# Optimization experiments

Hardware: AMD Instinct MI355X
Metric: run time of the kernel (lower is better)

The kernel has to match this reference:

```python
import jax, jax.numpy as jnp
import numpy as np

D = 64      # size_in
RANK = 4    # rank
N = 262144  # batch of samples


def setup_inputs() -> dict:
    key = jax.random.key(0)
    k1, k2, k3, k4, k5 = jax.random.split(key, 5)
    s1 = 1.0 / np.sqrt(D)        # torch Linear init bound for linear1 (in=D)
    s2 = 1.0 / np.sqrt(2 * D)    # bound for linear2 (in=2D)
    return {
        "t": jnp.zeros((1,), dtype=jnp.float32),
        "input_": jax.random.normal(k1, (N, 2 * D), dtype=jnp.float32),
        "W1": jax.random.uniform(k2, (2 * D, D), jnp.float32, -s1, s1),
        "b1": jax.random.uniform(k3, (2 * D,), jnp.float32, -s1, s1),
        "W2": jax.random.uniform(k4, (RANK * D, 2 * D), jnp.float32, -s2, s2),
        "b2": jax.random.uniform(k5, (RANK * D,), jnp.float32, -s2, s2),
    }


def reference(t, input_, W1, b1, W2, b2):
    # Per-sample scalar Hamiltonian H(inp) = sum_j (v . W[:, j])^2 where
    # W = tanh(linear2(tanh(linear1(x)))).reshape(D, RANK); the torch einsum
    # 'mij,mhj,mi,mh->m' factors as sum_j (sum_i W[i,j] v[i])^2.
    def H(inp):
        x, v = inp[:D], inp[D:]
        h = jnp.tanh(W1 @ x + b1)                       # [2D]
        Wm = jnp.tanh(W2 @ h + b2).reshape(D, RANK)     # [D, RANK]
        return jnp.sum((v @ Wm) ** 2)

    # batch_jacobian of a scalar-per-sample fn == per-sample gradient [N, 2D]
    g = jax.vmap(jax.grad(H))(input_)
    dx = g[:, :D]
    dv = -g[:, D:]
    return jnp.concatenate([dx, dv], axis=-1)
```

## Files before the change

kernel.cpp:

```cpp
#include <hip/hip_runtime.h>

#define DD    64
#define TWOD  128
#define RD    256
#define NT    3

typedef __attribute__((ext_vector_type(8))) short short8;
typedef __attribute__((ext_vector_type(4))) float float4v;
typedef __attribute__((ext_vector_type(4))) unsigned uint4v;
typedef unsigned long long ull;
typedef unsigned short ush;

__device__ __forceinline__ ush f2b(float f) {
    unsigned u = __builtin_bit_cast(unsigned, f);
    u += 0x7fffu + ((u >> 16) & 1u);
    return (ush)(u >> 16);
}
__device__ __forceinline__ float b2f(ush s) {
    unsigned u = ((unsigned)s) << 16;
    return __builtin_bit_cast(float, u);
}
__device__ __forceinline__ unsigned cvt_pk_bf16(float lo, float hi) {
    unsigned r;
    asm("v_cvt_pk_bf16_f32 %0, %1, %2" : "=v"(r) : "v"(lo), "v"(hi));
    return r;
}
__device__ __forceinline__ void store_pair(ush* p0, ush* p1, float lo, float hi) {
    unsigned pk = cvt_pk_bf16(lo, hi);
    *p0 = (ush)pk;
    *p1 = (ush)(pk >> 16);
}
__device__ __forceinline__ float ftanh(float x) {
    float e, r;
    asm("v_exp_f32 %0, %1" : "=v"(e) : "v"(x * 2.885390082f));
    asm("v_rcp_f32 %0, %1" : "=v"(r) : "v"(e + 1.0f));
    return __builtin_fmaf(-2.0f, r, 1.0f);
}
__device__ __forceinline__ void lds_fence() {
    asm volatile("s_waitcnt lgkmcnt(0)" ::: "memory");
}

__global__ void prep_weights(const float* __restrict__ W1, const float* __restrict__ W2,
                             ush* __restrict__ wa, ush* __restrict__ wd,
                             ush* __restrict__ wb, ush* __restrict__ wc) {
    int t = blockIdx.x * blockDim.x + threadIdx.x;
    if (t < 8192) {
        wa[t] = f2b(W1[t]);
        int c = t >> 7, r = t & 127;
        wd[t] = f2b(W1[r * 64 + c]);
    }
    if (t < 32768) {
        wb[t] = f2b(W2[t]);
        int c = t >> 8, k = t & 255;
        wc[t] = f2b(W2[k * 128 + c]);
    }
}

__global__ __launch_bounds__(64, 1) void geognn_kernel(
    const float* __restrict__ inp, const float* __restrict__ b1, const float* __restrict__ b2,
    const ush* __restrict__ wa, const ush* __restrict__ wd,
    const ush* __restrict__ wb, const ush* __restrict__ wc,
    float* __restrict__ out, long nrows) {

    __shared__ __align__(16) ush hd_s[NT][16 * 264];
    __shared__ ush v_s[NT][16][68];
    __shared__ float4v y_s[NT][16];

    const int  l   = threadIdx.x;
    const int  l15 = l & 15;
    const int  q   = l >> 4;
    long row0 = (long)blockIdx.x * (16 * NT);
    if (row0 + 16 * NT > nrows) row0 = nrows - 16 * NT;

#pragma unroll 1
    for (int r = 0; r < 16; r += 2) {
#pragma unroll
        for (int t = 0; t < NT; ++t) {
            float v0 = inp[(row0 + t * 16 + r)     * TWOD + DD + l];
            float v1 = inp[(row0 + t * 16 + r + 1) * TWOD + DD + l];
            store_pair(&v_s[t][r][l], &v_s[t][r + 1][l], v0, v1);
        }
    }

    short8 ax[NT][2];
#pragma unroll
    for (int t = 0; t < NT; ++t)
#pragma unroll
        for (int kb = 0; kb < 2; ++kb) {
            const float4v* p = (const float4v*)(inp + (row0 + t * 16 + l15) * TWOD + kb * 32 + q * 8);
            float4v f0 = p[0], f1 = p[1];
            uint4v pk = { cvt_pk_bf16(f0.x, f0.y), cvt_pk_bf16(f0.z, f0.w),
                          cvt_pk_bf16(f1.x, f1.y), cvt_pk_bf16(f1.z, f1.w) };
            ax[t][kb] = __builtin_bit_cast(short8, pk);
        }

    short8 awA[2], awB[2];
#pragma unroll
    for (int f = 0; f < 2; ++f)
        awA[f] = *(const short8*)(wa + (0 * 16 + l15) * DD + f * 32 + q * 8);

    auto g1step = [&](int nb, short8* cur, short8* nxt) {
        if (nb < 7) {
#pragma unroll
            for (int f = 0; f < 2; ++f)
                nxt[f] = *(const short8*)(wa + ((nb + 1) * 16 + l15) * DD + f * 32 + q * 8);
        }
        float bv = b1[nb * 16 + l15];
        const int c = nb * 16 + l15;
#pragma unroll
        for (int t = 0; t < NT; ++t) {
            float4v acc = {0.f, 0.f, 0.f, 0.f};
            acc = __builtin_amdgcn_mfma_f32_16x16x32_bf16(ax[t][0], cur[0], acc, 0, 0, 0);
            acc = __builtin_amdgcn_mfma_f32_16x16x32_bf16(ax[t][1], cur[1], acc, 0, 0, 0);
            float h0 = ftanh(acc[0] + bv);
            float h1 = ftanh(acc[1] + bv);
            float h2 = ftanh(acc[2] + bv);
            float h3 = ftanh(acc[3] + bv);
            store_pair(&hd_s[t][(q * 4 + 0) * 136 + c], &hd_s[t][(q * 4 + 1) * 136 + c], h0, h1);
            store_pair(&hd_s[t][(q * 4 + 2) * 136 + c], &hd_s[t][(q * 4 + 3) * 136 + c], h2, h3);
        }
    };
#pragma unroll 1
    for (int nbb = 0; nbb < 8; nbb += 2) {
        g1step(nbb,     awA, awB);
        g1step(nbb + 1, awB, awA);
    }

    short8 bwA[8], bwB[8];
#pragma unroll
    for (int f = 0; f < 8; ++f)
        bwA[f] = *(const short8*)(wb + ((f >> 2) * 16 + l15) * TWOD + (f & 3) * 32 + q * 8);

    lds_fence();

    short8 ha[NT][4];
#pragma unroll
    for (int t = 0; t < NT; ++t)
#pragma unroll
        for (int kb = 0; kb < 4; ++kb)
            ha[t][kb] = *(const short8*)(&hd_s[t][l15 * 136 + kb * 32 + q * 8]);

    lds_fence();

    float yp[NT][4] = {};
    auto g2step = [&](int p, short8* cur, short8* nxt) {
        if (p < 7) {
#pragma unroll
            for (int f = 0; f < 8; ++f)
                nxt[f] = *(const short8*)(wb + (((p + 1) * 2 + (f >> 2)) * 16 + l15) * TWOD
                                          + (f & 3) * 32 + q * 8);
        }
#pragma unroll
        for (int s = 0; s < 2; ++s) {
            const int nb = p * 2 + s;
            const int n  = nb * 16 + l15;
            const int c4 = nb * 4 + (l15 >> 2);
            float bv = b2[nb * 16 + l15];
#pragma unroll
            for (int t = 0; t < NT; ++t) {
                float4v acc = {0.f, 0.f, 0.f, 0.f};
#pragma unroll
                for (int kb = 0; kb < 4; ++kb)
                    acc = __builtin_amdgcn_mfma_f32_16x16x32_bf16(ha[t][kb], cur[s * 4 + kb], acc, 0, 0, 0);
                float u0 = ftanh(acc[0] + bv);
                float u1 = ftanh(acc[1] + bv);
                float u2 = ftanh(acc[2] + bv);
                float u3 = ftanh(acc[3] + bv);
                store_pair(&hd_s[t][(q * 4 + 0) * 264 + n], &hd_s[t][(q * 4 + 1) * 264 + n], u0, u1);
                store_pair(&hd_s[t][(q * 4 + 2) * 264 + n], &hd_s[t][(q * 4 + 3) * 264 + n], u2, u3);
                yp[t][0] += b2f(v_s[t][q * 4 + 0][c4]) * u0;
                yp[t][1] += b2f(v_s[t][q * 4 + 1][c4]) * u1;
                yp[t][2] += b2f(v_s[t][q * 4 + 2][c4]) * u2;
                yp[t][3] += b2f(v_s[t][q * 4 + 3][c4]) * u3;
            }
        }
    };
#pragma unroll 1
    for (int pp = 0; pp < 8; pp += 2) {
        g2step(pp,     bwA, bwB);
        g2step(pp + 1, bwB, bwA);
    }

#pragma unroll
    for (int t = 0; t < NT; ++t)
#pragma unroll
        for (int i = 0; i < 4; ++i) {
            yp[t][i] += __shfl_xor(yp[t][i], 4, 64);
            yp[t][i] += __shfl_xor(yp[t][i], 8, 64);
        }
    if (l15 < 4) {
#pragma unroll
        for (int t = 0; t < NT; ++t)
#pragma unroll
            for (int i = 0; i < 4; ++i)
                ((float*)&y_s[t][q * 4 + i])[l15] = yp[t][i];
    }

    short8 cwA[8], cwB[8];
#pragma unroll
    for (int kb = 0; kb < 8; ++kb)
        cwA[kb] = *(const short8*)(wc + l15 * RD + kb * 32 + q * 8);

    lds_fence();

#pragma unroll 1
    for (int r = 0; r < 16; ++r) {
#pragma unroll
        for (int t = 0; t < NT; ++t) {
            ull uu = *(const ull*)(&hd_s[t][r * 264 + 4 * l]);
            float4v y = y_s[t][r];
            float vv = b2f(v_s[t][r][l]);
            float u0 = b2f((ush)uu);
            float u1 = b2f((ush)(uu >> 16));
            float u2 = b2f((ush)(uu >> 32));
            float u3 = b2f((ush)(uu >> 48));
            float dvv = y.x * u0 + y.y * u1 + y.z * u2 + y.w * u3;
            out[(row0 + t * 16 + r) * TWOD + DD + l] = -2.0f * dvv;
            float t0 = 2.0f * y.x * vv * (1.0f - u0 * u0);
            float t1 = 2.0f * y.y * vv * (1.0f - u1 * u1);
            float t2 = 2.0f * y.z * vv * (1.0f - u2 * u2);
            float t3 = 2.0f * y.w * vv * (1.0f - u3 * u3);
            unsigned w0 = cvt_pk_bf16(t0, t1);
            unsigned w1 = cvt_pk_bf16(t2, t3);
            ull w = (ull)w0 | ((ull)w1 << 32);
            *(ull*)(&hd_s[t][r * 264 + 4 * l]) = w;
        }
    }

    lds_fence();

    short8 da[NT][8];
#pragma unroll
    for (int t = 0; t < NT; ++t)
#pragma unroll
        for (int kb = 0; kb < 8; ++kb)
            da[t][kb] = *(const short8*)(&hd_s[t][l15 * 264 + kb * 32 + q * 8]);

    lds_fence();

    auto g3step = [&](int nb, short8* cur, short8* nxt) {
        if (nb < 7) {
#pragma unroll
            for (int kb = 0; kb < 8; ++kb)
                nxt[kb] = *(const short8*)(wc + ((nb + 1) * 16 + l15) * RD + kb * 32 + q * 8);
        }
        const int c = nb * 16 + l15;
#pragma unroll
        for (int t = 0; t < NT; ++t) {
            float4v acc = {0.f, 0.f, 0.f, 0.f};
#pragma unroll
            for (int kb = 0; kb < 8; ++kb)
                acc = __builtin_amdgcn_mfma_f32_16x16x32_bf16(da[t][kb], cur[kb], acc, 0, 0, 0);
            store_pair(&hd_s[t][(q * 4 + 0) * 136 + c], &hd_s[t][(q * 4 + 1) * 136 + c], acc[0], acc[1]);
            store_pair(&hd_s[t][(q * 4 + 2) * 136 + c], &hd_s[t][(q * 4 + 3) * 136 + c], acc[2], acc[3]);
        }
    };
#pragma unroll 1
    for (int nbb = 0; nbb < 8; nbb += 2) {
        g3step(nbb,     cwA, cwB);
        g3step(nbb + 1, cwB, cwA);
    }

    lds_fence();

    short8 dw[16];
#pragma unroll
    for (int f = 0; f < 16; ++f)
        dw[f] = *(const short8*)(wd + ((f >> 2) * 16 + l15) * TWOD + (f & 3) * 32 + q * 8);

    short8 dfa[NT][4];
#pragma unroll
    for (int t = 0; t < NT; ++t)
#pragma unroll
        for (int kb = 0; kb < 4; ++kb) {
            short8 raw = *(const short8*)(&hd_s[t][l15 * 136 + kb * 32 + q * 8]);
            uint4v pk;
#pragma unroll
            for (int j = 0; j < 4; ++j) {
                float h0 = b2f((ush)ha[t][kb][2 * j]);
                float d0 = b2f((ush)raw[2 * j]);
                float h1 = b2f((ush)ha[t][kb][2 * j + 1]);
                float d1 = b2f((ush)raw[2 * j + 1]);
                float a0 = __builtin_fmaf(-(d0 * h0), h0, d0);
                float a1 = __builtin_fmaf(-(d1 * h1), h1, d1);
                pk[j] = cvt_pk_bf16(a0, a1);
            }
            dfa[t][kb] = __builtin_bit_cast(short8, pk);
        }
#pragma unroll
    for (int t = 0; t < NT; ++t)
#pragma unroll
        for (int nb = 0; nb < 4; ++nb) {
            float4v acc = {0.f, 0.f, 0.f, 0.f};
#pragma unroll
            for (int kb = 0; kb < 4; ++kb)
                acc = __builtin_amdgcn_mfma_f32_16x16x32_bf16(dfa[t][kb], dw[nb * 4 + kb], acc, 0, 0, 0);
#pragma unroll
            for (int i = 0; i < 4; ++i)
                out[(row0 + t * 16 + q * 4 + i) * TWOD + nb * 16 + l15] = acc[i];
        }
}

extern "C" void kernel_launch(void* const* d_in, const int* in_sizes, int n_in,
                              void* d_out, int out_size, void* d_ws, size_t ws_size,
                              hipStream_t stream) {
    const float* inp = (const float*)d_in[1];
    const float* W1  = (const float*)d_in[2];
    const float* b1  = (const float*)d_in[3];
    const float* W2  = (const float*)d_in[4];
    const float* b2  = (const float*)d_in[5];

    ush* wa = (ush*)d_ws;
    ush* wd = wa + 8192;
    ush* wb = wd + 8192;
    ush* wc = wb + 32768;

    prep_weights<<<128, 256, 0, stream>>>(W1, W2, wa, wd, wb, wc);

    const long rows = in_sizes[1] / TWOD;
    const int  grid = (int)((rows + 16 * NT - 1) / (16 * NT));
    geognn_kernel<<<grid, 64, 0, stream>>>(inp, b1, b2, wa, wd, wb, wc,
                                           (float*)d_out, rows);
}
```

Baseline: 391.9 us.

## Deepen weight prefetch to triple buffering and split LDS buffers for h and d

Weight tiles for the second and third GEMMs are now triple-buffered, loaded two steps ahead instead of one, and the step loops are fully unrolled. The first-layer weights are all loaded up front. The hidden activations get their own LDS buffer, which removes one fence and lets ha registers die before phase 3 (h is re-read from LDS later). The intent is to hide global-load latency behind the MFMA work, at the cost of more VGPRs and more LDS per block.

```diff
diff --git a/kernel.cpp b/kernel.cpp
--- a/kernel.cpp
+++ b/kernel.cpp
@@ -62,7 +62,8 @@
     const ush* __restrict__ wb, const ush* __restrict__ wc,
     float* __restrict__ out, long nrows) {
 
-    __shared__ __align__(16) ush hd_s[NT][16 * 264];
+    __shared__ __align__(16) ush h_s[NT][16 * 136];
+    __shared__ __align__(16) ush d_s[NT][16 * 264];
     __shared__ ush v_s[NT][16][68];
     __shared__ float4v y_s[NT][16];
 
@@ -72,15 +73,14 @@
     long row0 = (long)blockIdx.x * (16 * NT);
     if (row0 + 16 * NT > nrows) row0 = nrows - 16 * NT;
 
-#pragma unroll 1
-    for (int r = 0; r < 16; r += 2) {
-#pragma unroll
-        for (int t = 0; t < NT; ++t) {
+#pragma unroll
+    for (int t = 0; t < NT; ++t)
+#pragma unroll
+        for (int r = 0; r < 16; r += 2) {
             float v0 = inp[(row0 + t * 16 + r)     * TWOD + DD + l];
             float v1 = inp[(row0 + t * 16 + r + 1) * TWOD + DD + l];
             store_pair(&v_s[t][r][l], &v_s[t][r + 1][l], v0, v1);
         }
-    }
 
     short8 ax[NT][2];
 #pragma unroll
@@ -94,42 +94,37 @@
             ax[t][kb] = __builtin_bit_cast(short8, pk);
         }
 
-    short8 awA[2], awB[2];
-#pragma unroll
-    for (int f = 0; f < 2; ++f)
-        awA[f] = *(const short8*)(wa + (0 * 16 + l15) * DD + f * 32 + q * 8);
-
-    auto g1step = [&](int nb, short8* cur, short8* nxt) {
-        if (nb < 7) {
-#pragma unroll
-            for (int f = 0; f < 2; ++f)
-                nxt[f] = *(const short8*)(wa + ((nb + 1) * 16 + l15) * DD + f * 32 + q * 8);
-        }
+    short8 aw[16];
+#pragma unroll
+    for (int f = 0; f < 16; ++f)
+        aw[f] = *(const short8*)(wa + ((f >> 1) * 16 + l15) * DD + (f & 1) * 32 + q * 8);
+
+#pragma unroll
+    for (int nb = 0; nb < 8; ++nb) {
         float bv = b1[nb * 16 + l15];
         const int c = nb * 16 + l15;
 #pragma unroll
         for (int t = 0; t < NT; ++t) {
             float4v acc = {0.f, 0.f, 0.f, 0.f};
-            acc = __builtin_amdgcn_mfma_f32_16x16x32_bf16(ax[t][0], cur[0], acc, 0, 0, 0);
-            acc = __builtin_amdgcn_mfma_f32_16x16x32_bf16(ax[t][1], cur[1], acc, 0, 0, 0);
+            acc = __builtin_amdgcn_mfma_f32_16x16x32_bf16(ax[t][0], aw[nb * 2 + 0], acc, 0, 0, 0);
+            acc = __builtin_amdgcn_mfma_f32_16x16x32_bf16(ax[t][1], aw[nb * 2 + 1], acc, 0, 0, 0);
             float h0 = ftanh(acc[0] + bv);
             float h1 = ftanh(acc[1] + bv);
             float h2 = ftanh(acc[2] + bv);
             float h3 = ftanh(acc[3] + bv);
-            store_pair(&hd_s[t][(q * 4 + 0) * 136 + c], &hd_s[t][(q * 4 + 1) * 136 + c], h0, h1);
-            store_pair(&hd_s[t][(q * 4 + 2) * 136 + c], &hd_s[t][(q * 4 + 3) * 136 + c], h2, h3);
-        }
-    };
-#pragma unroll 1
-    for (int nbb = 0; nbb < 8; nbb += 2) {
-        g1step(nbb,     awA, awB);
-        g1step(nbb + 1, awB, awA);
+            store_pair(&h_s[t][(q * 4 + 0) * 136 + c], &h_s[t][(q * 4 + 1) * 136 + c], h0, h1);
+            store_pair(&h_s[t][(q * 4 + 2) * 136 + c], &h_s[t][(q * 4 + 3) * 136 + c], h2, h3);
+        }
     }
 
-    short8 bwA[8], bwB[8];
-#pragma unroll
-    for (int f = 0; f < 8; ++f)
-        bwA[f] = *(const short8*)(wb + ((f >> 2) * 16 + l15) * TWOD + (f & 3) * 32 + q * 8);
+    short8 bw0[8], bw1[8], bw2[8];
+#define WB_LOAD(buf, b)                                                              \
+    _Pragma("unroll")                                                                \
+    for (int f = 0; f < 8; ++f)                                                      \
+        buf[f] = *(const short8*)(wb + (((b) * 2 + (f >> 2)) * 16 + l15) * TWOD      \
+                                  + (f & 3) * 32 + q * 8);
+    WB_LOAD(bw0, 0)
+    WB_LOAD(bw1, 1)
 
     lds_fence();
 
@@ -138,18 +133,11 @@
     for (int t = 0; t < NT; ++t)
 #pragma unroll
         for (int kb = 0; kb < 4; ++kb)
-            ha[t][kb] = *(const short8*)(&hd_s[t][l15 * 136 + kb * 32 + q * 8]);
-
-    lds_fence();
+            ha[t][kb] = *(const short8*)(&h_s[t][l15 * 136 + kb * 32 + q * 8]);
 
     float yp[NT][4] = {};
     auto g2step = [&](int p, short8* cur, short8* nxt) {
-        if (p < 7) {
-#pragma unroll
-            for (int f = 0; f < 8; ++f)
-                nxt[f] = *(const short8*)(wb + (((p + 1) * 2 + (f >> 2)) * 16 + l15) * TWOD
-                                          + (f & 3) * 32 + q * 8);
-        }
+        if (nxt) { WB_LOAD(nxt, p + 2) }
 #pragma unroll
         for (int s = 0; s < 2; ++s) {
             const int nb = p * 2 + s;
@@ -166,8 +154,8 @@
                 float u1 = ftanh(acc[1] + bv);
                 float u2 = ftanh(acc[2] + bv);
                 float u3 = ftanh(acc[3] + bv);
-                store_pair(&hd_s[t][(q * 4 + 0) * 264 + n], &hd_s[t][(q * 4 + 1) * 264 + n], u0, u1);
-                store_pair(&hd_s[t][(q * 4 + 2) * 264 + n], &hd_s[t][(q * 4 + 3) * 264 + n], u2, u3);
+                store_pair(&d_s[t][(q * 4 + 0) * 264 + n], &d_s[t][(q * 4 + 1) * 264 + n], u0, u1);
+                store_pair(&d_s[t][(q * 4 + 2) * 264 + n], &d_s[t][(q * 4 + 3) * 264 + n], u2, u3);
                 yp[t][0] += b2f(v_s[t][q * 4 + 0][c4]) * u0;
                 yp[t][1] += b2f(v_s[t][q * 4 + 1][c4]) * u1;
                 yp[t][2] += b2f(v_s[t][q * 4 + 2][c4]) * u2;
@@ -175,11 +163,14 @@
             }
         }
     };
-#pragma unroll 1
-    for (int pp = 0; pp < 8; pp += 2) {
-        g2step(pp,     bwA, bwB);
-        g2step(pp + 1, bwB, bwA);
-    }
+    g2step(0, bw0, bw2);
+    g2step(1, bw1, bw0);
+    g2step(2, bw2, bw1);
+    g2step(3, bw0, bw2);
+    g2step(4, bw1, bw0);
+    g2step(5, bw2, bw1);
+    g2step(6, bw0, nullptr);
+    g2step(7, bw1, nullptr);
 
 #pragma unroll
     for (int t = 0; t < NT; ++t)
@@ -196,18 +187,21 @@
                 ((float*)&y_s[t][q * 4 + i])[l15] = yp[t][i];
     }
 
-    short8 cwA[8], cwB[8];
-#pragma unroll
-    for (int kb = 0; kb < 8; ++kb)
-        cwA[kb] = *(const short8*)(wc + l15 * RD + kb * 32 + q * 8);
-
-    lds_fence();
-
-#pragma unroll 1
-    for (int r = 0; r < 16; ++r) {
-#pragma unroll
-        for (int t = 0; t < NT; ++t) {
-            ull uu = *(const ull*)(&hd_s[t][r * 264 + 4 * l]);
+    short8 cw0[8], cw1[8], cw2[8];
+#define WC_LOAD(buf, b)                                                              \
+    _Pragma("unroll")                                                                \
+    for (int kb = 0; kb < 8; ++kb)                                                   \
+        buf[kb] = *(const short8*)(wc + ((b) * 16 + l15) * RD + kb * 32 + q * 8);
+    WC_LOAD(cw0, 0)
+    WC_LOAD(cw1, 1)
+
+    lds_fence();
+
+#pragma unroll
+    for (int t = 0; t < NT; ++t)
+#pragma unroll
+        for (int r = 0; r < 16; ++r) {
+            ull uu = *(const ull*)(&d_s[t][r * 264 + 4 * l]);
             float4v y = y_s[t][r];
             float vv = b2f(v_s[t][r][l]);
             float u0 = b2f((ush)uu);
@@ -223,9 +217,8 @@
             unsigned w0 = cvt_pk_bf16(t0, t1);
             unsigned w1 = cvt_pk_bf16(t2, t3);
             ull w = (ull)w0 | ((ull)w1 << 32);
-            *(ull*)(&hd_s[t][r * 264 + 4 * l]) = w;
-        }
-    }
+            *(ull*)(&d_s[t][r * 264 + 4 * l]) = w;
+        }
 
     lds_fence();
 
@@ -234,16 +227,12 @@
     for (int t = 0; t < NT; ++t)
 #pragma unroll
         for (int kb = 0; kb < 8; ++kb)
-            da[t][kb] = *(const short8*)(&hd_s[t][l15 * 264 + kb * 32 + q * 8]);
+            da[t][kb] = *(const short8*)(&d_s[t][l15 * 264 + kb * 32 + q * 8]);
 
     lds_fence();
 
     auto g3step = [&](int nb, short8* cur, short8* nxt) {
-        if (nb < 7) {
-#pragma unroll
-            for (int kb = 0; kb < 8; ++kb)
-                nxt[kb] = *(const short8*)(wc + ((nb + 1) * 16 + l15) * RD + kb * 32 + q * 8);
-        }
+        if (nxt) { WC_LOAD(nxt, nb + 2) }
         const int c = nb * 16 + l15;
 #pragma unroll
         for (int t = 0; t < NT; ++t) {
@@ -251,36 +240,40 @@
 #pragma unroll
             for (int kb = 0; kb < 8; ++kb)
                 acc = __builtin_amdgcn_mfma_f32_16x16x32_bf16(da[t][kb], cur[kb], acc, 0, 0, 0);
-            store_pair(&hd_s[t][(q * 4 + 0) * 136 + c], &hd_s[t][(q * 4 + 1) * 136 + c], acc[0], acc[1]);
-            store_pair(&hd_s[t][(q * 4 + 2) * 136 + c], &hd_s[t][(q * 4 + 3) * 136 + c], acc[2], acc[3]);
+            store_pair(&d_s[t][(q * 4 + 0) * 136 + c], &d_s[t][(q * 4 + 1) * 136 + c], acc[0], acc[1]);
+            store_pair(&d_s[t][(q * 4 + 2) * 136 + c], &d_s[t][(q * 4 + 3) * 136 + c], acc[2], acc[3]);
         }
     };
-#pragma unroll 1
-    for (int nbb = 0; nbb < 8; nbb += 2) {
-        g3step(nbb,     cwA, cwB);
-        g3step(nbb + 1, cwB, cwA);
-    }
-
-    lds_fence();
+    g3step(0, cw0, cw2);
+    g3step(1, cw1, cw0);
+    g3step(2, cw2, cw1);
+    g3step(3, cw0, cw2);
+    g3step(4, cw1, cw0);
+    g3step(5, cw2, cw1);
+    g3step(6, cw0, nullptr);
+    g3step(7, cw1, nullptr);
 
     short8 dw[16];
 #pragma unroll
     for (int f = 0; f < 16; ++f)
         dw[f] = *(const short8*)(wd + ((f >> 2) * 16 + l15) * TWOD + (f & 3) * 32 + q * 8);
 
+    lds_fence();
+
     short8 dfa[NT][4];
 #pragma unroll
     for (int t = 0; t < NT; ++t)
 #pragma unroll
         for (int kb = 0; kb < 4; ++kb) {
-            short8 raw = *(const short8*)(&hd_s[t][l15 * 136 + kb * 32 + q * 8]);
+            short8 rawd = *(const short8*)(&d_s[t][l15 * 136 + kb * 32 + q * 8]);
+            short8 rawh = *(const short8*)(&h_s[t][l15 * 136 + kb * 32 + q * 8]);
             uint4v pk;
 #pragma unroll
             for (int j = 0; j < 4; ++j) {
-                float h0 = b2f((ush)ha[t][kb][2 * j]);
-                float d0 = b2f((ush)raw[2 * j]);
-                float h1 = b2f((ush)ha[t][kb][2 * j + 1]);
-                float d1 = b2f((ush)raw[2 * j + 1]);
+                float d0 = b2f((ush)rawd[2 * j]);
+                float h0 = b2f((ush)rawh[2 * j]);
+                float d1 = b2f((ush)rawd[2 * j + 1]);
+                float h1 = b2f((ush)rawh[2 * j + 1]);
                 float a0 = __builtin_fmaf(-(d0 * h0), h0, d0);
                 float a1 = __builtin_fmaf(-(d1 * h1), h1, d1);
                 pk[j] = cvt_pk_bf16(a0, a1);
@@ -299,6 +292,8 @@
             for (int i = 0; i < 4; ++i)
                 out[(row0 + t * 16 + q * 4 + i) * TWOD + nb * 16 + l15] = acc[i];
         }
+#undef WB_LOAD
+#undef WC_LOAD
 }
 
 extern "C" void kernel_launch(void* const* d_in, const int* in_sizes, int n_in,
```

Result: faster. 356.5 us (-9.0%).
